# Kernel tuning notes

Hardware: AMD Instinct MI355X
Metric: run time of the kernel (lower is better)

The kernel has to match this reference:

```python
import jax, jax.numpy as jnp
import numpy as np

N_NODES, N_EDGES, N_GRAPHS = 100000, 400000, 4096
F_NODE, F_EDGE, G = 78, 11, 256
NUM_LAYERS, NUM_TIMESTEPS = 3, 2
L = NUM_LAYERS - 1  # number of GNNLayers after GetContext


def _lrelu(x):
    return jax.nn.leaky_relu(x, 0.01)


def _seg_softmax(logits, seg, n):
    # softmax of logits grouped by segment id (edge_softmax over dst / softmax_nodes over graph)
    m = jax.ops.segment_max(logits, seg, num_segments=n)
    e = jnp.exp(logits - m[seg])
    s = jax.ops.segment_sum(e, seg, num_segments=n)
    return e / s[seg]


def _gru(x, h, Wih, Whh, bih, bhh):
    gi = x @ Wih.T + bih
    gh = h @ Whh.T + bhh
    ir, iz, inn = jnp.split(gi, 3, axis=-1)
    hr, hz, hn = jnp.split(gh, 3, axis=-1)
    r = jax.nn.sigmoid(ir + hr)
    z = jax.nn.sigmoid(iz + hz)
    nn_ = jnp.tanh(inn + r * hn)
    return (1.0 - z) * nn_ + z * h


def _forward(node_feats, edge_feats, W_pn, b_pn, W_pe1, b_pe1, W_pe2, b_pe2, W_et, b_et,
             gru0_Wih, gru0_Whh, gru0_bih, gru0_bhh,
             gnn_W_pe, gnn_b_pe, gnn_W_pn, gnn_b_pn, gnn_Wih, gnn_Whh, gnn_bih, gnn_bhh,
             ro_W_cl, ro_b_cl, ro_W_pn, ro_b_pn, ro_Wih, ro_Whh, ro_bih, ro_bhh,
             ln_gamma, ln_beta, src, dst, node_graph):
    N, B = node_feats.shape[0], N_GRAPHS
    # ---- GetContext ----
    hv_new = _lrelu(node_feats @ W_pn.T + b_pn)                                  # [N,G]
    he1 = _lrelu(jnp.concatenate([node_feats[src], edge_feats], -1) @ W_pe1.T + b_pe1)  # [E,G]
    logits = _lrelu(jnp.concatenate([hv_new[dst], he1], -1) @ W_pe2.T + b_pe2)   # [E,1]
    a = _seg_softmax(logits, dst, N)
    c = jax.ops.segment_sum(a * (he1 @ W_et.T + b_et), dst, num_segments=N)      # [N,G]
    h = jax.nn.relu(_gru(jax.nn.elu(c), hv_new, gru0_Wih, gru0_Whh, gru0_bih, gru0_bhh))
    # ---- GNNLayers (AttentiveGRU2) ----
    for l in range(L):
        lg = _lrelu(jnp.concatenate([h[dst], h[src]], -1) @ gnn_W_pe[l].T + gnn_b_pe[l])  # [E,1]
        a = _seg_softmax(lg, dst, N)
        hv = h @ gnn_W_pn[l].T + gnn_b_pn[l]
        c = jax.ops.segment_sum(a * hv[src], dst, num_segments=N)
        h = jax.nn.relu(_gru(jax.nn.elu(c), h, gnn_Wih[l], gnn_Whh[l], gnn_bih[l], gnn_bhh[l]))
    # ---- AttentiveFPReadout ----
    g_feats = jax.ops.segment_sum(h, node_graph, num_segments=B)                 # [B,G]
    for t in range(NUM_TIMESTEPS):
        z = _lrelu(jnp.concatenate([jax.nn.relu(g_feats)[node_graph], h], -1) @ ro_W_cl[t].T + ro_b_cl[t])  # [N,1]
        a = _seg_softmax(z, node_graph, B)
        hv = h @ ro_W_pn[t].T + ro_b_pn[t]
        gr = jax.ops.segment_sum(a * hv, node_graph, num_segments=B)
        g_feats = jax.nn.relu(_gru(jax.nn.elu(gr), g_feats, ro_Wih[t], ro_Whh[t], ro_bih[t], ro_bhh[t]))
    # ---- LayerNorm (dropout is identity at inference) ----
    mu = jnp.mean(g_feats, -1, keepdims=True)
    var = jnp.mean((g_feats - mu) ** 2, -1, keepdims=True)
    return (g_feats - mu) / jnp.sqrt(var + 1e-5) * ln_gamma + ln_beta


def setup_inputs() -> dict:
    key = jax.random.key(0)
    ks = iter(jax.random.split(key, 64))

    def nrm(shape, scale=1.0):
        return jax.random.normal(next(ks), shape, dtype=jnp.float32) * scale

    def lin(out_d, in_d):
        return nrm((out_d, in_d), 1.0 / np.sqrt(in_d))

    d = {}
    d['node_feats'] = nrm((N_NODES, F_NODE))
    d['edge_feats'] = nrm((N_EDGES, F_EDGE))
    d['src'] = jax.random.randint(next(ks), (N_EDGES,), 0, N_NODES)
    d['dst'] = jax.random.randint(next(ks), (N_EDGES,), 0, N_NODES)
    d['node_graph'] = jnp.sort(jax.random.randint(next(ks), (N_NODES,), 0, N_GRAPHS))
    # GetContext params
    d['W_pn'] = lin(G, F_NODE); d['b_pn'] = jnp.zeros((G,), jnp.float32)
    d['W_pe1'] = lin(G, F_NODE + F_EDGE); d['b_pe1'] = jnp.zeros((G,), jnp.float32)
    d['W_pe2'] = lin(1, 2 * G); d['b_pe2'] = jnp.zeros((1,), jnp.float32)
    d['W_et'] = lin(G, G); d['b_et'] = jnp.zeros((G,), jnp.float32)
    d['gru0_Wih'] = lin(3 * G, G); d['gru0_Whh'] = lin(3 * G, G)
    d['gru0_bih'] = jnp.zeros((3 * G,), jnp.float32); d['gru0_bhh'] = jnp.zeros((3 * G,), jnp.float32)
    # stacked GNNLayer params
    s2g = 1.0 / np.sqrt(2 * G); sg = 1.0 / np.sqrt(G)
    d['gnn_W_pe'] = nrm((L, 1, 2 * G), s2g); d['gnn_b_pe'] = jnp.zeros((L, 1), jnp.float32)
    d['gnn_W_pn'] = nrm((L, G, G), sg); d['gnn_b_pn'] = jnp.zeros((L, G), jnp.float32)
    d['gnn_Wih'] = nrm((L, 3 * G, G), sg); d['gnn_Whh'] = nrm((L, 3 * G, G), sg)
    d['gnn_bih'] = jnp.zeros((L, 3 * G), jnp.float32); d['gnn_bhh'] = jnp.zeros((L, 3 * G), jnp.float32)
    # stacked readout (GlobalPool) params
    T = NUM_TIMESTEPS
    d['ro_W_cl'] = nrm((T, 1, 2 * G), s2g); d['ro_b_cl'] = jnp.zeros((T, 1), jnp.float32)
    d['ro_W_pn'] = nrm((T, G, G), sg); d['ro_b_pn'] = jnp.zeros((T, G), jnp.float32)
    d['ro_Wih'] = nrm((T, 3 * G, G), sg); d['ro_Whh'] = nrm((T, 3 * G, G), sg)
    d['ro_bih'] = jnp.zeros((T, 3 * G), jnp.float32); d['ro_bhh'] = jnp.zeros((T, 3 * G), jnp.float32)
    d['ln_gamma'] = jnp.ones((G,), jnp.float32); d['ln_beta'] = jnp.zeros((G,), jnp.float32)
    return d


def reference(node_feats, edge_feats, src, dst, node_graph, W_pn, b_pn, W_pe1, b_pe1, W_pe2, b_pe2,
              W_et, b_et, gru0_Wih, gru0_Whh, gru0_bih, gru0_bhh,
              gnn_W_pe, gnn_b_pe, gnn_W_pn, gnn_b_pn, gnn_Wih, gnn_Whh, gnn_bih, gnn_bhh,
              ro_W_cl, ro_b_cl, ro_W_pn, ro_b_pn, ro_Wih, ro_Whh, ro_bih, ro_bhh, ln_gamma, ln_beta):
    return _forward(node_feats, edge_feats, W_pn, b_pn, W_pe1, b_pe1, W_pe2, b_pe2, W_et, b_et,
                    gru0_Wih, gru0_Whh, gru0_bih, gru0_bhh,
                    gnn_W_pe, gnn_b_pe, gnn_W_pn, gnn_b_pn, gnn_Wih, gnn_Whh, gnn_bih, gnn_bhh,
                    ro_W_cl, ro_b_cl, ro_W_pn, ro_b_pn, ro_Wih, ro_Whh, ro_bih, ro_bhh,
                    ln_gamma, ln_beta, src, dst, node_graph)
```

## Files before the change

kernel.cpp:

```cpp
#include <hip/hip_runtime.h>

#define NN 100000
#define NE 400000
#define NB 4096
#define FN 78
#define FE 11
#define GD 256
#define NL 2
#define NT 2

typedef unsigned short u16;
typedef __attribute__((ext_vector_type(8))) short bf16x8;
typedef __attribute__((ext_vector_type(4))) float f32x4;

__device__ __forceinline__ float lrelu_(float x){ return x > 0.f ? x : 0.01f*x; }
__device__ __forceinline__ float elu_(float x){ return x > 0.f ? x : expf(x) - 1.f; }
__device__ __forceinline__ float sigm_(float x){ return 1.f/(1.f + expf(-x)); }

__device__ __forceinline__ float bf2f(u16 u){ return __uint_as_float(((unsigned)u) << 16); }
__device__ __forceinline__ u16 f2bf(float f){
  unsigned u = __float_as_uint(f);
  unsigned r = (u + 0x7fffu + ((u >> 16) & 1u)) >> 16;
  return (u16)r;
}
__device__ __forceinline__ float ldv(const float* p, size_t i){ return p[i]; }
__device__ __forceinline__ float ldv(const u16* p, size_t i){ return bf2f(p[i]); }
__device__ __forceinline__ void stv(float* p, size_t i, float v){ p[i] = v; }
__device__ __forceinline__ void stv(u16* p, size_t i, float v){ p[i] = f2bf(v); }

__global__ void k_zero(float* p, size_t n){
  size_t i = (size_t)blockIdx.x*blockDim.x + threadIdx.x;
  size_t st = (size_t)gridDim.x*blockDim.x;
  for (; i < n; i += st) p[i] = 0.f;
}

__global__ void k_count(const int* __restrict__ dst, int* __restrict__ cnt, int E){
  int e = blockIdx.x*256 + threadIdx.x;
  if (e < E) atomicAdd(&cnt[dst[e]], 1);
}
__global__ void k_scan1(const int* __restrict__ cnt, int* __restrict__ part,
                        int* __restrict__ btot, int n){
  __shared__ int sd[256];
  int i = blockIdx.x*256 + threadIdx.x;
  int v = (i < n) ? cnt[i] : 0;
  sd[threadIdx.x] = v; __syncthreads();
  for (int d=1; d<256; d<<=1){
    int t = (threadIdx.x >= d) ? sd[threadIdx.x-d] : 0;
    __syncthreads();
    sd[threadIdx.x] += t;
    __syncthreads();
  }
  if (i < n) part[i] = sd[threadIdx.x];
  if (threadIdx.x == 255) btot[blockIdx.x] = sd[255];
}
__global__ void k_scan2(const int* __restrict__ btot, int* __restrict__ boff, int nb){
  __shared__ int sd[512];
  int tid = threadIdx.x;
  int v = (tid < nb) ? btot[tid] : 0;
  sd[tid] = v; __syncthreads();
  for (int d=1; d<512; d<<=1){
    int t = (tid >= d) ? sd[tid-d] : 0;
    __syncthreads();
    sd[tid] += t;
    __syncthreads();
  }
  if (tid < nb) boff[tid] = sd[tid] - v;
}
__global__ void k_scan3(const int* __restrict__ part, const int* __restrict__ boff,
                        int* __restrict__ rowptr, int n){
  int i = blockIdx.x*256 + threadIdx.x;
  if (i < n) rowptr[i+1] = part[i] + boff[blockIdx.x];
  if (i == 0) rowptr[0] = 0;
}
__global__ void k_cursor(const int* __restrict__ rowptr, int* __restrict__ cursor, int n){
  int i = blockIdx.x*256 + threadIdx.x;
  if (i < n) cursor[i] = rowptr[i];
}
__global__ void k_fill(const int* __restrict__ dst, int* __restrict__ cursor,
                       int* __restrict__ order, int E){
  int e = blockIdx.x*256 + threadIdx.x;
  if (e < E){
    int pos = atomicAdd(&cursor[dst[e]], 1);
    order[pos] = e;
  }
}
__global__ void k_gpb(const int* __restrict__ ng, int* __restrict__ gpb, int N, int B){
  int b = blockIdx.x*256 + threadIdx.x;
  if (b > B) return;
  int lo = 0, hi = N;
  while (lo < hi){ int mid = (lo+hi)>>1; if (ng[mid] < b) lo = mid+1; else hi = mid; }
  gpb[b] = lo;
}

__global__ void k_pack_b(const float* __restrict__ W, u16* __restrict__ Bp, int OUT, int K){
  int t = blockIdx.x*256 + threadIdx.x;
  if (t >= OUT*K) return;
  int j = t & 7;
  int l = (t >> 3) & 63;
  int rest = t >> 9;
  int nks = K >> 5;
  int ks = rest % nks, c = rest / nks;
  int col = c*16 + (l & 15);
  int k = ks*32 + (l >> 4)*8 + j;
  Bp[t] = f2bf(W[(size_t)col*K + k]);
}

template<int TN>
__global__ void k_node_proj(const float* __restrict__ nf, const float* __restrict__ W, int ldw,
                            const float* __restrict__ b, int act, u16* __restrict__ outb, int N){
  __shared__ float sx[TN][FN];
  int base = blockIdx.x*TN, tid = threadIdx.x;
  for (int i = tid; i < TN*FN; i += 256){
    int n = i / FN, k = i % FN;
    int row = base + n;
    sx[n][k] = (row < N) ? nf[(size_t)row*FN + k] : 0.f;
  }
  __syncthreads();
  int j = tid;
  float acc[TN];
  #pragma unroll
  for (int n=0;n<TN;n++) acc[n]=0.f;
  for (int k=0;k<FN;k++){
    float w = W[(size_t)j*ldw + k];
    #pragma unroll
    for (int n=0;n<TN;n++) acc[n] += w*sx[n][k];
  }
  float bb = b ? b[j] : 0.f;
  #pragma unroll
  for (int n=0;n<TN;n++){
    int row = base + n;
    if (row < N){
      float v = acc[n] + bb;
      outb[(size_t)row*GD + j] = f2bf(act ? lrelu_(v) : v);
    }
  }
}

__global__ void k_dot2_bf16(const u16* __restrict__ rows, const float* __restrict__ wv,
                            float* __restrict__ za, float* __restrict__ zb, int N){
  int wav = threadIdx.x >> 6, lane = threadIdx.x & 63;
  int i = blockIdx.x*4 + wav;
  if (i >= N) return;
  int c0 = lane*4;
  ushort4 r4 = *(const ushort4*)&rows[(size_t)i*GD + c0];
  float4 wa = *(const float4*)&wv[c0];
  float4 wb = *(const float4*)&wv[GD + c0];
  float v0 = bf2f(r4.x), v1 = bf2f(r4.y), v2 = bf2f(r4.z), v3 = bf2f(r4.w);
  float va = v0*wa.x + v1*wa.y + v2*wa.z + v3*wa.w;
  float vb = v0*wb.x + v1*wb.y + v2*wb.z + v3*wb.w;
  #pragma unroll
  for (int off=32; off; off>>=1){ va += __shfl_down(va, off); vb += __shfl_down(vb, off); }
  if (lane == 0){ za[i] = va; zb[i] = vb; }
}

__global__ void k_dot1_bf16(const u16* __restrict__ rows, const float* __restrict__ wv,
                            float* __restrict__ z, int N){
  int wav = threadIdx.x >> 6, lane = threadIdx.x & 63;
  int i = blockIdx.x*4 + wav;
  if (i >= N) return;
  int c0 = lane*4;
  ushort4 r4 = *(const ushort4*)&rows[(size_t)i*GD + c0];
  float4 wa = *(const float4*)&wv[c0];
  float va = bf2f(r4.x)*wa.x + bf2f(r4.y)*wa.y + bf2f(r4.z)*wa.z + bf2f(r4.w)*wa.w;
  #pragma unroll
  for (int off=32; off; off>>=1) va += __shfl_down(va, off);
  if (lane == 0) z[i] = va;
}

__global__ void k_dotg_relu(const float* __restrict__ g, const float* __restrict__ wv,
                            float* __restrict__ zg, int B){
  int wav = threadIdx.x >> 6, lane = threadIdx.x & 63;
  int i = blockIdx.x*4 + wav;
  if (i >= B) return;
  int c0 = lane*4;
  float4 gv = *(const float4*)&g[(size_t)i*GD + c0];
  float4 wa = *(const float4*)&wv[c0];
  float va = fmaxf(gv.x,0.f)*wa.x + fmaxf(gv.y,0.f)*wa.y + fmaxf(gv.z,0.f)*wa.z + fmaxf(gv.w,0.f)*wa.w;
  #pragma unroll
  for (int off=32; off; off>>=1) va += __shfl_down(va, off);
  if (lane == 0) zg[i] = va;
}

__global__ void __launch_bounds__(256)
k_ctx_fused(const u16* __restrict__ P, const float* __restrict__ za,
            const int* __restrict__ order, const int* __restrict__ rowptr,
            const int* __restrict__ src, const float* __restrict__ ef,
            const float* __restrict__ Wpe1, const float* __restrict__ bpe1,
            const float* __restrict__ Wpe2, const float* __restrict__ bpe2,
            u16* __restrict__ wc, float* __restrict__ sdeg, int N){
  int wv = threadIdx.x >> 6, lane = threadIdx.x & 63;
  int d = blockIdx.x*4 + wv;
  if (d >= N) return;
  int j0 = rowptr[d], j1 = rowptr[d+1];
  int c0 = lane*4;
  float wb0 = Wpe2[GD+c0], wb1 = Wpe2[GD+c0+1], wb2 = Wpe2[GD+c0+2], wb3 = Wpe2[GD+c0+3];
  float bp0 = bpe1[c0], bp1 = bpe1[c0+1], bp2 = bpe1[c0+2], bp3 = bpe1[c0+3];
  float wk0[FE], wk1[FE], wk2[FE], wk3[FE];
  #pragma unroll
  for (int k=0;k<FE;k++){
    wk0[k] = Wpe1[(size_t)(c0+0)*(FN+FE) + FN + k];
    wk1[k] = Wpe1[(size_t)(c0+1)*(FN+FE) + FN + k];
    wk2[k] = Wpe1[(size_t)(c0+2)*(FN+FE) + FN + k];
    wk3[k] = Wpe1[(size_t)(c0+3)*(FN+FE) + FN + k];
  }
  float zad = za[d] + bpe2[0];
  float m = -1e30f, s = 0.f;
  float a0=0.f, a1=0.f, a2=0.f, a3=0.f;
  for (int j=j0; j<j1; j++){
    int e = order[j];
    int sn = src[e];
    ushort4 p4 = *(const ushort4*)&P[(size_t)sn*GD + c0];
    const float* efp = &ef[(size_t)e*FE];
    float efv[FE];
    #pragma unroll
    for (int k=0;k<FE;k++) efv[k] = efp[k];
    float h0 = bf2f(p4.x)+bp0, h1 = bf2f(p4.y)+bp1, h2 = bf2f(p4.z)+bp2, h3 = bf2f(p4.w)+bp3;
    #pragma unroll
    for (int k=0;k<FE;k++){
      h0 += wk0[k]*efv[k]; h1 += wk1[k]*efv[k]; h2 += wk2[k]*efv[k]; h3 += wk3[k]*efv[k];
    }
    h0 = lrelu_(h0); h1 = lrelu_(h1); h2 = lrelu_(h2); h3 = lrelu_(h3);
    float part = h0*wb0 + h1*wb1 + h2*wb2 + h3*wb3;
    #pragma unroll
    for (int off=32; off; off>>=1) part += __shfl_down(part, off);
    float l = lrelu_(part + zad);
    l = __shfl(l, 0);
    float mn = fmaxf(m, l);
    float sc = __expf(m - mn);
    float p  = __expf(l - mn);
    s = s*sc + p;
    a0 = a0*sc + p*h0; a1 = a1*sc + p*h1; a2 = a2*sc + p*h2; a3 = a3*sc + p*h3;
    m = mn;
  }
  float inv = (j1 > j0) ? 1.f/s : 0.f;
  ushort4 o;
  o.x = f2bf(a0*inv); o.y = f2bf(a1*inv); o.z = f2bf(a2*inv); o.w = f2bf(a3*inv);
  *(ushort4*)&wc[(size_t)d*GD + c0] = o;
  if (lane == 0) sdeg[d] = (j1 > j0) ? 1.f : 0.f;
}

__global__ void __launch_bounds__(256)
k_gnn_fused(const u16* __restrict__ hv, const float* __restrict__ za, const float* __restrict__ zb,
            const int* __restrict__ order, const int* __restrict__ rowptr,
            const int* __restrict__ src, const float* __restrict__ bias,
            u16* __restrict__ cw, int N){
  int wv = threadIdx.x >> 6, lane = threadIdx.x & 63;
  int d = blockIdx.x*4 + wv;
  if (d >= N) return;
  int j0 = rowptr[d], j1 = rowptr[d+1];
  int c0 = lane*4;
  float zad = za[d] + bias[0];
  float m = -1e30f, s = 0.f;
  float a0=0.f, a1=0.f, a2=0.f, a3=0.f;
  for (int j=j0; j<j1; j++){
    int e = order[j];
    int sn = src[e];
    float l = lrelu_(zad + zb[sn]);
    ushort4 r4 = *(const ushort4*)&hv[(size_t)sn*GD + c0];
    float mn = fmaxf(m, l);
    float sc = __expf(m - mn);
    float p  = __expf(l - mn);
    s = s*sc + p;
    a0 = a0*sc + p*bf2f(r4.x);
    a1 = a1*sc + p*bf2f(r4.y);
    a2 = a2*sc + p*bf2f(r4.z);
    a3 = a3*sc + p*bf2f(r4.w);
    m = mn;
  }
  float inv = (j1 > j0) ? 1.f/s : 0.f;
  ushort4 o;
  o.x = f2bf(a0*inv); o.y = f2bf(a1*inv); o.z = f2bf(a2*inv); o.w = f2bf(a3*inv);
  *(ushort4*)&cw[(size_t)d*GD + c0] = o;
}

__global__ void __launch_bounds__(256)
k_ro_fused(const u16* __restrict__ hv, const float* __restrict__ zg, const float* __restrict__ zh,
           const int* __restrict__ gpb, const float* __restrict__ bias,
           float* __restrict__ gr, int B){
  int b = blockIdx.x, tid = threadIdx.x;
  int i0 = gpb[b], i1 = gpb[b+1];
  float zgb = zg[b] + bias[0];
  __shared__ float red[256];
  float lm = -1e30f;
  for (int i = i0 + tid; i < i1; i += 256) lm = fmaxf(lm, lrelu_(zgb + zh[i]));
  red[tid] = lm; __syncthreads();
  for (int d2=128; d2; d2>>=1){ if (tid < d2) red[tid] = fmaxf(red[tid], red[tid+d2]); __syncthreads(); }
  float M = red[0]; __syncthreads();
  float ls = 0.f;
  for (int i = i0 + tid; i < i1; i += 256) ls += __expf(lrelu_(zgb + zh[i]) - M);
  red[tid] = ls; __syncthreads();
  for (int d2=128; d2; d2>>=1){ if (tid < d2) red[tid] += red[tid+d2]; __syncthreads(); }
  float S = red[0];
  float acc = 0.f;
  for (int i = i0; i < i1; i++){
    float p = __expf(lrelu_(zgb + zh[i]) - M);
    acc += p * bf2f(hv[(size_t)i*GD + tid]);
  }
  gr[(size_t)b*GD + tid] = (i1 > i0) ? acc/S : 0.f;
}

__global__ void k_segsum_sorted(const u16* __restrict__ h, const int* __restrict__ gpb,
                                float* __restrict__ g, int B){
  int b = blockIdx.x, tid = threadIdx.x;
  int i0 = gpb[b], i1 = gpb[b+1];
  float acc = 0.f;
  for (int i = i0; i < i1; i++) acc += bf2f(h[(size_t)i*GD + tid]);
  g[(size_t)b*GD + tid] = acc;
}

template<typename XT, typename HT, typename OT>
__global__ void __launch_bounds__(256)
k_gru_mfma(const XT* __restrict__ x, const HT* __restrict__ hprev,
           const u16* __restrict__ Wihp, const u16* __restrict__ Whhp,
           const float* __restrict__ bih, const float* __restrict__ bhh,
           OT* __restrict__ hout, int R, const float* __restrict__ xmask){
  int tid = threadIdx.x;
  int wave = tid >> 6, lane = tid & 63;
  int m = lane & 15, kg = lane >> 4;
  int r0 = blockIdx.x*16;

  f32x4 agi[3][4], agh[3][4];
  #pragma unroll
  for (int g=0;g<3;g++)
    #pragma unroll
    for (int t=0;t<4;t++){ agi[g][t] = (f32x4)(0.f); agh[g][t] = (f32x4)(0.f); }

  float mk = xmask ? (xmask[r0 + m] > 0.f ? 1.f : 0.f) : 1.f;
  #pragma unroll
  for (int ks=0; ks<8; ks++){
    int koff = ks*32 + kg*8;
    float xr[8];
    if constexpr (sizeof(XT) == 2){
      bf16x8 xw = *(const bf16x8*)&x[(size_t)(r0 + m)*GD + koff];
      #pragma unroll
      for (int q=0;q<8;q++) xr[q] = bf2f((u16)xw[q]);
    } else {
      const float* xp = (const float*)x + (size_t)(r0 + m)*GD + koff;
      float4 x0 = *(const float4*)xp;
      float4 x1 = *(const float4*)(xp+4);
      xr[0]=x0.x; xr[1]=x0.y; xr[2]=x0.z; xr[3]=x0.w;
      xr[4]=x1.x; xr[5]=x1.y; xr[6]=x1.z; xr[7]=x1.w;
    }
    bf16x8 ax;
    #pragma unroll
    for (int q=0;q<8;q++) ax[q] = (short)f2bf(elu_(xr[q]*mk));
    bf16x8 ah;
    if constexpr (sizeof(HT) == 2){
      ah = *(const bf16x8*)&hprev[(size_t)(r0 + m)*GD + koff];
    } else {
      const float* hr = (const float*)hprev + (size_t)(r0 + m)*GD + koff;
      float4 h0 = *(const float4*)hr;
      float4 h1 = *(const float4*)(hr+4);
      ah[0]=(short)f2bf(h0.x); ah[1]=(short)f2bf(h0.y); ah[2]=(short)f2bf(h0.z); ah[3]=(short)f2bf(h0.w);
      ah[4]=(short)f2bf(h1.x); ah[5]=(short)f2bf(h1.y); ah[6]=(short)f2bf(h1.z); ah[7]=(short)f2bf(h1.w);
    }
    #pragma unroll
    for (int g=0;g<3;g++){
      #pragma unroll
      for (int t=0;t<4;t++){
        int c = g*16 + wave*4 + t;
        bf16x8 bi = *(const bf16x8*)&Wihp[(size_t)((c*8 + ks)*64 + lane)*8];
        bf16x8 bh = *(const bf16x8*)&Whhp[(size_t)((c*8 + ks)*64 + lane)*8];
        agi[g][t] = __builtin_amdgcn_mfma_f32_16x16x32_bf16(ax, bi, agi[g][t], 0, 0, 0);
        agh[g][t] = __builtin_amdgcn_mfma_f32_16x16x32_bf16(ah, bh, agh[g][t], 0, 0, 0);
      }
    }
  }
  #pragma unroll
  for (int t=0;t<4;t++){
    int col = wave*64 + t*16 + m;
    float bir = bih[col],     bhr = bhh[col];
    float biz = bih[col+GD],  bhz = bhh[col+GD];
    float bin = bih[col+2*GD],bhn = bhh[col+2*GD];
    #pragma unroll
    for (int i=0;i<4;i++){
      int row = r0 + kg*4 + i;
      float rr = sigm_(agi[0][t][i] + bir + agh[0][t][i] + bhr);
      float zz = sigm_(agi[1][t][i] + biz + agh[1][t][i] + bhz);
      float nn = tanhf(agi[2][t][i] + bin + rr*(agh[2][t][i] + bhn));
      float hp = ldv(hprev, (size_t)row*GD + col);
      float o = (1.f - zz)*nn + zz*hp;
      stv(hout, (size_t)row*GD + col, fmaxf(o, 0.f));
    }
  }
}

__global__ void __launch_bounds__(256)
k_proj_mfma(const u16* __restrict__ X, const u16* __restrict__ Wp,
            const float* __restrict__ b, u16* __restrict__ Y, int R){
  int tid = threadIdx.x;
  int wave = tid >> 6, lane = tid & 63;
  int m = lane & 15, kg = lane >> 4;
  int r0 = blockIdx.x*32;
  f32x4 acc[2][4];
  #pragma unroll
  for (int rf=0;rf<2;rf++)
    #pragma unroll
    for (int t=0;t<4;t++) acc[rf][t] = (f32x4)(0.f);
  #pragma unroll
  for (int ks=0; ks<8; ks++){
    int koff = ks*32 + kg*8;
    bf16x8 a0 = *(const bf16x8*)&X[(size_t)(r0 + m)*GD + koff];
    bf16x8 a1 = *(const bf16x8*)&X[(size_t)(r0 + 16 + m)*GD + koff];
    #pragma unroll
    for (int t=0;t<4;t++){
      int c = wave*4 + t;
      bf16x8 bv = *(const bf16x8*)&Wp[(size_t)((c*8 + ks)*64 + lane)*8];
      acc[0][t] = __builtin_amdgcn_mfma_f32_16x16x32_bf16(a0, bv, acc[0][t], 0, 0, 0);
      acc[1][t] = __builtin_amdgcn_mfma_f32_16x16x32_bf16(a1, bv, acc[1][t], 0, 0, 0);
    }
  }
  #pragma unroll
  for (int t=0;t<4;t++){
    int col = wave*64 + t*16 + m;
    float bb = b[col];
    #pragma unroll
    for (int rf=0;rf<2;rf++){
      #pragma unroll
      for (int i=0;i<4;i++){
        int row = r0 + rf*16 + kg*4 + i;
        Y[(size_t)row*GD + col] = f2bf(acc[rf][t][i] + bb);
      }
    }
  }
}

__global__ void k_layernorm(const float* __restrict__ gb, const float* __restrict__ gamma,
                            const float* __restrict__ beta, float* __restrict__ outb){
  int r = blockIdx.x, j = threadIdx.x;
  float v = gb[(size_t)r*GD + j];
  float s1 = v, s2 = v*v;
  #pragma unroll
  for (int off=32; off; off>>=1){ s1 += __shfl_down(s1, off); s2 += __shfl_down(s2, off); }
  __shared__ float r1[4], r2[4];
  int wv = j >> 6, lane = j & 63;
  if (lane == 0){ r1[wv] = s1; r2[wv] = s2; }
  __syncthreads();
  float S1 = r1[0]+r1[1]+r1[2]+r1[3];
  float S2 = r2[0]+r2[1]+r2[2]+r2[3];
  float mu = S1/(float)GD;
  float var = fmaxf(S2/(float)GD - mu*mu, 0.f);
  outb[(size_t)r*GD + j] = (v - mu)/sqrtf(var + 1e-5f)*gamma[j] + beta[j];
}

extern "C" void kernel_launch(void* const* d_in, const int* in_sizes, int n_in,
                              void* d_out, int out_size, void* d_ws, size_t ws_size,
                              hipStream_t stream){
  const float* node_feats = (const float*)d_in[0];
  const float* edge_feats = (const float*)d_in[1];
  const int*   src        = (const int*)d_in[2];
  const int*   dst        = (const int*)d_in[3];
  const int*   node_graph = (const int*)d_in[4];
  const float* W_pn   = (const float*)d_in[5];
  const float* b_pn   = (const float*)d_in[6];
  const float* W_pe1  = (const float*)d_in[7];
  const float* b_pe1  = (const float*)d_in[8];
  const float* W_pe2  = (const float*)d_in[9];
  const float* b_pe2  = (const float*)d_in[10];
  const float* W_et   = (const float*)d_in[11];
  const float* b_et   = (const float*)d_in[12];
  const float* g0_Wih = (const float*)d_in[13];
  const float* g0_Whh = (const float*)d_in[14];
  const float* g0_bih = (const float*)d_in[15];
  const float* g0_bhh = (const float*)d_in[16];
  const float* gnn_W_pe = (const float*)d_in[17];
  const float* gnn_b_pe = (const float*)d_in[18];
  const float* gnn_W_pn = (const float*)d_in[19];
  const float* gnn_b_pn = (const float*)d_in[20];
  const float* gnn_Wih  = (const float*)d_in[21];
  const float* gnn_Whh  = (const float*)d_in[22];
  const float* gnn_bih  = (const float*)d_in[23];
  const float* gnn_bhh  = (const float*)d_in[24];
  const float* ro_W_cl = (const float*)d_in[25];
  const float* ro_b_cl = (const float*)d_in[26];
  const float* ro_W_pn = (const float*)d_in[27];
  const float* ro_b_pn = (const float*)d_in[28];
  const float* ro_Wih  = (const float*)d_in[29];
  const float* ro_Whh  = (const float*)d_in[30];
  const float* ro_bih  = (const float*)d_in[31];
  const float* ro_bhh  = (const float*)d_in[32];
  const float* ln_gamma = (const float*)d_in[33];
  const float* ln_beta  = (const float*)d_in[34];
  float* outp = (float*)d_out;

  const int NBLK = (NN + 255)/256;

  char* w = (char*)d_ws;
  size_t need = 0;
  float* gbuf  = (float*)(w + need); need += (size_t)NB*GD*4;
  float* grbuf = (float*)(w + need); need += (size_t)NB*GD*4;
  float* za    = (float*)(w + need); need += (size_t)NN*4;
  float* zb    = (float*)(w + need); need += (size_t)NN*4;
  float* zg    = (float*)(w + need); need += (size_t)NB*4;
  float* sdeg  = (float*)(w + need); need += (size_t)NN*4;
  int*   cnt    = (int*)(w + need); need += (size_t)NN*4;
  int*   rowptr = (int*)(w + need); need += (size_t)(NN+1)*4;
  int*   cursor = (int*)(w + need); need += (size_t)NN*4;
  int*   order  = (int*)(w + need); need += (size_t)NE*4;
  int*   gpb    = (int*)(w + need); need += (size_t)(NB+1)*4;
  int*   btot   = (int*)(w + need); need += (size_t)512*4;
  int*   boff   = (int*)(w + need); need += (size_t)512*4;
  u16*   hbuf = (u16*)(w + need); need += (size_t)NN*GD*2;
  u16*   htmp = (u16*)(w + need); need += (size_t)NN*GD*2;
  u16*   cwb  = (u16*)(w + need); need += (size_t)NN*GD*2;
  u16*   dbuf = (u16*)(w + need); need += (size_t)NN*GD*2;
  u16* pGru = (u16*)(w + need); need += (size_t)10*768*GD*2;
  u16* pPn  = (u16*)(w + need); need += (size_t)4*GD*GD*2;
  u16* pEt  = (u16*)(w + need); need += (size_t)GD*GD*2;
  if (ws_size < need) return;
  u16* Pbuf   = hbuf;
  u16* hv_new = htmp;

  const size_t GW = (size_t)768*GD;
  const size_t PW = (size_t)GD*GD;

  k_zero<<<64, 256, 0, stream>>>((float*)cnt, (size_t)NN);
  k_count<<<(NE+255)/256, 256, 0, stream>>>(dst, cnt, NE);
  k_scan1<<<NBLK, 256, 0, stream>>>(cnt, cnt, btot, NN);
  k_scan2<<<1, 512, 0, stream>>>(btot, boff, NBLK);
  k_scan3<<<NBLK, 256, 0, stream>>>(cnt, boff, rowptr, NN);
  k_cursor<<<NBLK, 256, 0, stream>>>(rowptr, cursor, NN);
  k_fill<<<(NE+255)/256, 256, 0, stream>>>(dst, cursor, order, NE);
  k_gpb<<<(NB+256)/256, 256, 0, stream>>>(node_graph, gpb, NN, NB);

  k_pack_b<<<768, 256, 0, stream>>>(g0_Wih, pGru + 0*GW, 768, GD);
  k_pack_b<<<768, 256, 0, stream>>>(g0_Whh, pGru + 1*GW, 768, GD);
  for (int l=0;l<NL;l++){
    k_pack_b<<<768, 256, 0, stream>>>(gnn_Wih + (size_t)l*3*GD*GD, pGru + (2+2*l)*GW, 768, GD);
    k_pack_b<<<768, 256, 0, stream>>>(gnn_Whh + (size_t)l*3*GD*GD, pGru + (3+2*l)*GW, 768, GD);
    k_pack_b<<<256, 256, 0, stream>>>(gnn_W_pn + (size_t)l*GD*GD, pPn + l*PW, GD, GD);
  }
  for (int t=0;t<NT;t++){
    k_pack_b<<<768, 256, 0, stream>>>(ro_Wih + (size_t)t*3*GD*GD, pGru + (6+2*t)*GW, 768, GD);
    k_pack_b<<<768, 256, 0, stream>>>(ro_Whh + (size_t)t*3*GD*GD, pGru + (7+2*t)*GW, 768, GD);
    k_pack_b<<<256, 256, 0, stream>>>(ro_W_pn + (size_t)t*GD*GD, pPn + (2+t)*PW, GD, GD);
  }
  k_pack_b<<<256, 256, 0, stream>>>(W_et, pEt, GD, GD);

  k_node_proj<8><<<(NN+7)/8, 256, 0, stream>>>(node_feats, W_pn, FN, b_pn, 1, hv_new, NN);
  k_node_proj<8><<<(NN+7)/8, 256, 0, stream>>>(node_feats, W_pe1, FN+FE, nullptr, 0, Pbuf, NN);
  k_dot1_bf16<<<(NN+3)/4, 256, 0, stream>>>(hv_new, W_pe2, za, NN);
  k_ctx_fused<<<(NN+3)/4, 256, 0, stream>>>(Pbuf, za, order, rowptr, src, edge_feats,
                                            W_pe1, b_pe1, W_pe2, b_pe2, cwb, sdeg, NN);
  k_proj_mfma<<<NN/32, 256, 0, stream>>>(cwb, pEt, b_et, dbuf, NN);
  k_gru_mfma<u16,u16,u16><<<NN/16, 256, 0, stream>>>(dbuf, hv_new, pGru + 0*GW, pGru + 1*GW,
                                                     g0_bih, g0_bhh, hbuf, NN, sdeg);

  for (int l=0; l<NL; l++){
    k_dot2_bf16<<<(NN+3)/4, 256, 0, stream>>>(hbuf, gnn_W_pe + (size_t)l*2*GD, za, zb, NN);
    k_proj_mfma<<<NN/32, 256, 0, stream>>>(hbuf, pPn + l*PW, gnn_b_pn + (size_t)l*GD, htmp, NN);
    k_gnn_fused<<<(NN+3)/4, 256, 0, stream>>>(htmp, za, zb, order, rowptr, src,
                                              gnn_b_pe + l, cwb, NN);
    k_gru_mfma<u16,u16,u16><<<NN/16, 256, 0, stream>>>(cwb, hbuf,
                                pGru + (2+2*l)*GW, pGru + (3+2*l)*GW,
                                gnn_bih + (size_t)l*3*GD, gnn_bhh + (size_t)l*3*GD, hbuf, NN, nullptr);
  }

  k_segsum_sorted<<<NB, 256, 0, stream>>>(hbuf, gpb, gbuf, NB);
  for (int t=0; t<NT; t++){
    k_dotg_relu<<<(NB+3)/4, 256, 0, stream>>>(gbuf, ro_W_cl + (size_t)t*2*GD, zg, NB);
    k_dot1_bf16<<<(NN+3)/4, 256, 0, stream>>>(hbuf, ro_W_cl + (size_t)t*2*GD + GD, za, NN);
    k_proj_mfma<<<NN/32, 256, 0, stream>>>(hbuf, pPn + (2+t)*PW, ro_b_pn + (size_t)t*GD, htmp, NN);
    k_ro_fused<<<NB, 256, 0, stream>>>(htmp, zg, za, gpb, ro_b_cl + t, grbuf, NB);
    k_gru_mfma<float,float,float><<<NB/16, 256, 0, stream>>>(grbuf, gbuf,
                                pGru + (6+2*t)*GW, pGru + (7+2*t)*GW,
                                ro_bih + (size_t)t*3*GD, ro_bhh + (size_t)t*3*GD, gbuf, NB, nullptr);
  }
  k_layernorm<<<NB, 256, 0, stream>>>(gbuf, ln_gamma, ln_beta, outp);
}
```

Measured before the change: 2.220 ms.

## Tile GRU and projection MFMA kernels to 64 rows and move ELU into producers

The node-level GRU and projection kernels now process 64 rows per 512-thread block instead of 16 or 32, so each loaded weight fragment feeds four row-tile MFMAs rather than one or two. This is meant to cut repeated weight reads from cache, which were issued once per small block. The ELU (and the degree mask on the context path) moves out of the GRU prologue into the epilogues that produce its input: the GNN aggregation kernel and a templated projection kernel. The trade-off is many more accumulator registers per thread, which may limit occupancy or cause spills, and the last partial tile is handled by clamping reads and guarding writes.

```diff
diff --git a/kernel.cpp b/kernel.cpp
--- a/kernel.cpp
+++ b/kernel.cpp
@@ -23,10 +23,6 @@
   unsigned r = (u + 0x7fffu + ((u >> 16) & 1u)) >> 16;
   return (u16)r;
 }
-__device__ __forceinline__ float ldv(const float* p, size_t i){ return p[i]; }
-__device__ __forceinline__ float ldv(const u16* p, size_t i){ return bf2f(p[i]); }
-__device__ __forceinline__ void stv(float* p, size_t i, float v){ p[i] = v; }
-__device__ __forceinline__ void stv(u16* p, size_t i, float v){ p[i] = f2bf(v); }
 
 __global__ void k_zero(float* p, size_t n){
   size_t i = (size_t)blockIdx.x*blockDim.x + threadIdx.x;
@@ -269,7 +265,8 @@
   }
   float inv = (j1 > j0) ? 1.f/s : 0.f;
   ushort4 o;
-  o.x = f2bf(a0*inv); o.y = f2bf(a1*inv); o.z = f2bf(a2*inv); o.w = f2bf(a3*inv);
+  o.x = f2bf(elu_(a0*inv)); o.y = f2bf(elu_(a1*inv));
+  o.z = f2bf(elu_(a2*inv)); o.w = f2bf(elu_(a3*inv));
   *(ushort4*)&cw[(size_t)d*GD + c0] = o;
 }
 
@@ -308,12 +305,134 @@
   g[(size_t)b*GD + tid] = acc;
 }
 
-template<typename XT, typename HT, typename OT>
+__global__ void __launch_bounds__(512)
+k_gru_mfma64(const u16* __restrict__ x, const u16* __restrict__ hprev,
+             const u16* __restrict__ Wihp, const u16* __restrict__ Whhp,
+             const float* __restrict__ bih, const float* __restrict__ bhh,
+             u16* __restrict__ hout, int R){
+  int tid = threadIdx.x;
+  int wv = tid >> 6, lane = tid & 63;
+  int m = lane & 15, kg = lane >> 4;
+  int r0 = blockIdx.x*64;
+
+  f32x4 agi[3][2][4], agh[3][2][4];
+  #pragma unroll
+  for (int g=0;g<3;g++)
+    #pragma unroll
+    for (int t=0;t<2;t++)
+      #pragma unroll
+      for (int rt=0;rt<4;rt++){ agi[g][t][rt] = (f32x4)(0.f); agh[g][t][rt] = (f32x4)(0.f); }
+
+  #pragma unroll
+  for (int ks=0; ks<8; ks++){
+    int koff = ks*32 + kg*8;
+    bf16x8 ax[4], ah[4];
+    #pragma unroll
+    for (int rt=0; rt<4; rt++){
+      int row = r0 + rt*16 + m;
+      if (row > R-1) row = R-1;
+      ax[rt] = *(const bf16x8*)&x[(size_t)row*GD + koff];
+      ah[rt] = *(const bf16x8*)&hprev[(size_t)row*GD + koff];
+    }
+    #pragma unroll
+    for (int g=0;g<3;g++){
+      #pragma unroll
+      for (int t=0;t<2;t++){
+        int c = g*16 + wv*2 + t;
+        bf16x8 bi = *(const bf16x8*)&Wihp[(size_t)((c*8 + ks)*64 + lane)*8];
+        bf16x8 bh = *(const bf16x8*)&Whhp[(size_t)((c*8 + ks)*64 + lane)*8];
+        #pragma unroll
+        for (int rt=0; rt<4; rt++){
+          agi[g][t][rt] = __builtin_amdgcn_mfma_f32_16x16x32_bf16(ax[rt], bi, agi[g][t][rt], 0, 0, 0);
+          agh[g][t][rt] = __builtin_amdgcn_mfma_f32_16x16x32_bf16(ah[rt], bh, agh[g][t][rt], 0, 0, 0);
+        }
+      }
+    }
+  }
+  #pragma unroll
+  for (int t=0;t<2;t++){
+    int col = wv*32 + t*16 + m;
+    float bir = bih[col],      bhr = bhh[col];
+    float biz = bih[col+GD],   bhz = bhh[col+GD];
+    float bin = bih[col+2*GD], bhn = bhh[col+2*GD];
+    #pragma unroll
+    for (int rt=0; rt<4; rt++){
+      #pragma unroll
+      for (int i=0;i<4;i++){
+        int row = r0 + rt*16 + kg*4 + i;
+        if (row < R){
+          float rr = sigm_(agi[0][t][rt][i] + bir + agh[0][t][rt][i] + bhr);
+          float zz = sigm_(agi[1][t][rt][i] + biz + agh[1][t][rt][i] + bhz);
+          float nn = tanhf(agi[2][t][rt][i] + bin + rr*(agh[2][t][rt][i] + bhn));
+          float hp = bf2f(hprev[(size_t)row*GD + col]);
+          float o = (1.f - zz)*nn + zz*hp;
+          hout[(size_t)row*GD + col] = f2bf(fmaxf(o, 0.f));
+        }
+      }
+    }
+  }
+}
+
+template<int DO_ELU>
+__global__ void __launch_bounds__(512)
+k_proj_mfma64(const u16* __restrict__ X, const u16* __restrict__ Wp,
+              const float* __restrict__ b, u16* __restrict__ Y, int R,
+              const float* __restrict__ mask){
+  int tid = threadIdx.x;
+  int wv = tid >> 6, lane = tid & 63;
+  int m = lane & 15, kg = lane >> 4;
+  int r0 = blockIdx.x*64;
+  f32x4 acc[2][4];
+  #pragma unroll
+  for (int t=0;t<2;t++)
+    #pragma unroll
+    for (int rt=0;rt<4;rt++) acc[t][rt] = (f32x4)(0.f);
+  #pragma unroll
+  for (int ks=0; ks<8; ks++){
+    int koff = ks*32 + kg*8;
+    bf16x8 a[4];
+    #pragma unroll
+    for (int rt=0; rt<4; rt++){
+      int row = r0 + rt*16 + m;
+      if (row > R-1) row = R-1;
+      a[rt] = *(const bf16x8*)&X[(size_t)row*GD + koff];
+    }
+    #pragma unroll
+    for (int t=0;t<2;t++){
+      int c = wv*2 + t;
+      bf16x8 bv = *(const bf16x8*)&Wp[(size_t)((c*8 + ks)*64 + lane)*8];
+      #pragma unroll
+      for (int rt=0; rt<4; rt++)
+        acc[t][rt] = __builtin_amdgcn_mfma_f32_16x16x32_bf16(a[rt], bv, acc[t][rt], 0, 0, 0);
+    }
+  }
+  #pragma unroll
+  for (int t=0;t<2;t++){
+    int col = wv*32 + t*16 + m;
+    float bb = b[col];
+    #pragma unroll
+    for (int rt=0; rt<4; rt++){
+      #pragma unroll
+      for (int i=0;i<4;i++){
+        int row = r0 + rt*16 + kg*4 + i;
+        if (row < R){
+          float v = acc[t][rt][i] + bb;
+          if (DO_ELU){
+            float mk = (mask[row] > 0.f) ? 1.f : 0.f;
+            v = elu_(v*mk);
+          }
+          Y[(size_t)row*GD + col] = f2bf(v);
+        }
+      }
+    }
+  }
+}
+
 __global__ void __launch_bounds__(256)
-k_gru_mfma(const XT* __restrict__ x, const HT* __restrict__ hprev,
-           const u16* __restrict__ Wihp, const u16* __restrict__ Whhp,
-           const float* __restrict__ bih, const float* __restrict__ bhh,
-           OT* __restrict__ hout, int R, const float* __restrict__ xmask){
+k_gru_mfma_f32(const float* __restrict__ x, const float* __restrict__ hprev,
+               const u16* __restrict__ Wihp, const u16* __restrict__ Whhp,
+               const float* __restrict__ bih, const float* __restrict__ bhh,
+               float* __restrict__ hout, int R){
   int tid = threadIdx.x;
   int wave = tid >> 6, lane = tid & 63;
   int m = lane & 15, kg = lane >> 4;
@@ -325,35 +444,23 @@
     #pragma unroll
     for (int t=0;t<4;t++){ agi[g][t] = (f32x4)(0.f); agh[g][t] = (f32x4)(0.f); }
 
-  float mk = xmask ? (xmask[r0 + m] > 0.f ? 1.f : 0.f) : 1.f;
   #pragma unroll
   for (int ks=0; ks<8; ks++){
     int koff = ks*32 + kg*8;
-    float xr[8];
-    if constexpr (sizeof(XT) == 2){
-      bf16x8 xw = *(const bf16x8*)&x[(size_t)(r0 + m)*GD + koff];
-      #pragma unroll
-      for (int q=0;q<8;q++) xr[q] = bf2f((u16)xw[q]);
-    } else {
-      const float* xp = (const float*)x + (size_t)(r0 + m)*GD + koff;
-      float4 x0 = *(const float4*)xp;
-      float4 x1 = *(const float4*)(xp+4);
-      xr[0]=x0.x; xr[1]=x0.y; xr[2]=x0.z; xr[3]=x0.w;
-      xr[4]=x1.x; xr[5]=x1.y; xr[6]=x1.z; xr[7]=x1.w;
-    }
+    const float* xp = x + (size_t)(r0 + m)*GD + koff;
+    float4 x0 = *(const float4*)xp;
+    float4 x1 = *(const float4*)(xp+4);
     bf16x8 ax;
-    #pragma unroll
-    for (int q=0;q<8;q++) ax[q] = (short)f2bf(elu_(xr[q]*mk));
+    ax[0]=(short)f2bf(elu_(x0.x)); ax[1]=(short)f2bf(elu_(x0.y));
+    ax[2]=(short)f2bf(elu_(x0.z)); ax[3]=(short)f2bf(elu_(x0.w));
+    ax[4]=(short)f2bf(elu_(x1.x)); ax[5]=(short)f2bf(elu_(x1.y));
+    ax[6]=(short)f2bf(elu_(x1.z)); ax[7]=(short)f2bf(elu_(x1.w));
+    const float* hr = hprev + (size_t)(r0 + m)*GD + koff;
+    float4 h0 = *(const float4*)hr;
+    float4 h1 = *(const float4*)(hr+4);
     bf16x8 ah;
-    if constexpr (sizeof(HT) == 2){
-      ah = *(const bf16x8*)&hprev[(size_t)(r0 + m)*GD + koff];
-    } else {
-      const float* hr = (const float*)hprev + (size_t)(r0 + m)*GD + koff;
-      float4 h0 = *(const float4*)hr;
-      float4 h1 = *(const float4*)(hr+4);
-      ah[0]=(short)f2bf(h0.x); ah[1]=(short)f2bf(h0.y); ah[2]=(short)f2bf(h0.z); ah[3]=(short)f2bf(h0.w);
-      ah[4]=(short)f2bf(h1.x); ah[5]=(short)f2bf(h1.y); ah[6]=(short)f2bf(h1.z); ah[7]=(short)f2bf(h1.w);
-    }
+    ah[0]=(short)f2bf(h0.x); ah[1]=(short)f2bf(h0.y); ah[2]=(short)f2bf(h0.z); ah[3]=(short)f2bf(h0.w);
+    ah[4]=(short)f2bf(h1.x); ah[5]=(short)f2bf(h1.y); ah[6]=(short)f2bf(h1.z); ah[7]=(short)f2bf(h1.w);
     #pragma unroll
     for (int g=0;g<3;g++){
       #pragma unroll
@@ -369,58 +476,18 @@
   #pragma unroll
   for (int t=0;t<4;t++){
     int col = wave*64 + t*16 + m;
-    float bir = bih[col],     bhr = bhh[col];
-    float biz = bih[col+GD],  bhz = bhh[col+GD];
-    float bin = bih[col+2*GD],bhn = bhh[col+2*GD];
+    float bir = bih[col],      bhr = bhh[col];
+    float biz = bih[col+GD],   bhz = bhh[col+GD];
+    float bin = bih[col+2*GD], bhn = bhh[col+2*GD];
     #pragma unroll
     for (int i=0;i<4;i++){
       int row = r0 + kg*4 + i;
       float rr = sigm_(agi[0][t][i] + bir + agh[0][t][i] + bhr);
       float zz = sigm_(agi[1][t][i] + biz + agh[1][t][i] + bhz);
       float nn = tanhf(agi[2][t][i] + bin + rr*(agh[2][t][i] + bhn));
-      float hp = ldv(hprev, (size_t)row*GD + col);
+      float hp = hprev[(size_t)row*GD + col];
       float o = (1.f - zz)*nn + zz*hp;
-      stv(hout, (size_t)row*GD + col, fmaxf(o, 0.f));
-    }
-  }
-}
-
-__global__ void __launch_bounds__(256)
-k_proj_mfma(const u16* __restrict__ X, const u16* __restrict__ Wp,
-            const float* __restrict__ b, u16* __restrict__ Y, int R){
-  int tid = threadIdx.x;
-  int wave = tid >> 6, lane = tid & 63;
-  int m = lane & 15, kg = lane >> 4;
-  int r0 = blockIdx.x*32;
-  f32x4 acc[2][4];
-  #pragma unroll
-  for (int rf=0;rf<2;rf++)
-    #pragma unroll
-    for (int t=0;t<4;t++) acc[rf][t] = (f32x4)(0.f);
-  #pragma unroll
-  for (int ks=0; ks<8; ks++){
-    int koff = ks*32 + kg*8;
-    bf16x8 a0 = *(const bf16x8*)&X[(size_t)(r0 + m)*GD + koff];
-    bf16x8 a1 = *(const bf16x8*)&X[(size_t)(r0 + 16 + m)*GD + koff];
-    #pragma unroll
-    for (int t=0;t<4;t++){
-      int c = wave*4 + t;
-      bf16x8 bv = *(const bf16x8*)&Wp[(size_t)((c*8 + ks)*64 + lane)*8];
-      acc[0][t] = __builtin_amdgcn_mfma_f32_16x16x32_bf16(a0, bv, acc[0][t], 0, 0, 0);
-      acc[1][t] = __builtin_amdgcn_mfma_f32_16x16x32_bf16(a1, bv, acc[1][t], 0, 0, 0);
-    }
-  }
-  #pragma unroll
-  for (int t=0;t<4;t++){
-    int col = wave*64 + t*16 + m;
-    float bb = b[col];
-    #pragma unroll
-    for (int rf=0;rf<2;rf++){
-      #pragma unroll
-      for (int i=0;i<4;i++){
-        int row = r0 + rf*16 + kg*4 + i;
-        Y[(size_t)row*GD + col] = f2bf(acc[rf][t][i] + bb);
-      }
+      hout[(size_t)row*GD + col] = fmaxf(o, 0.f);
     }
   }
 }
@@ -513,6 +580,7 @@
 
   const size_t GW = (size_t)768*GD;
   const size_t PW = (size_t)GD*GD;
+  const int G64 = (NN + 63)/64;
 
   k_zero<<<64, 256, 0, stream>>>((float*)cnt, (size_t)NN);
   k_count<<<(NE+255)/256, 256, 0, stream>>>(dst, cnt, NE);
@@ -542,29 +610,31 @@
   k_dot1_bf16<<<(NN+3)/4, 256, 0, stream>>>(hv_new, W_pe2, za, NN);
   k_ctx_fused<<<(NN+3)/4, 256, 0, stream>>>(Pbuf, za, order, rowptr, src, edge_feats,
                                             W_pe1, b_pe1, W_pe2, b_pe2, cwb, sdeg, NN);
-  k_proj_mfma<<<NN/32, 256, 0, stream>>>(cwb, pEt, b_et, dbuf, NN);
-  k_gru_mfma<u16,u16,u16><<<NN/16, 256, 0, stream>>>(dbuf, hv_new, pGru + 0*GW, pGru + 1*GW,
-                                                     g0_bih, g0_bhh, hbuf, NN, sdeg);
+  k_proj_mfma64<1><<<G64, 512, 0, stream>>>(cwb, pEt, b_et, dbuf, NN, sdeg);
+  k_gru_mfma64<<<G64, 512, 0, stream>>>(dbuf, hv_new, pGru + 0*GW, pGru + 1*GW,
+                                        g0_bih, g0_bhh, hbuf, NN);
 
   for (int l=0; l<NL; l++){
     k_dot2_bf16<<<(NN+3)/4, 256, 0, stream>>>(hbuf, gnn_W_pe + (size_t)l*2*GD, za, zb, NN);
-    k_proj_mfma<<<NN/32, 256, 0, stream>>>(hbuf, pPn + l*PW, gnn_b_pn + (size_t)l*GD, htmp, NN);
+    k_proj_mfma64<0><<<G64, 512, 0, stream>>>(hbuf, pPn + l*PW, gnn_b_pn + (size_t)l*GD,
+                                              htmp, NN, nullptr);
     k_gnn_fused<<<(NN+3)/4, 256, 0, stream>>>(htmp, za, zb, order, rowptr, src,
                                               gnn_b_pe + l, cwb, NN);
-    k_gru_mfma<u16,u16,u16><<<NN/16, 256, 0, stream>>>(cwb, hbuf,
+    k_gru_mfma64<<<G64, 512, 0, stream>>>(cwb, hbuf,
                                 pGru + (2+2*l)*GW, pGru + (3+2*l)*GW,
-                                gnn_bih + (size_t)l*3*GD, gnn_bhh + (size_t)l*3*GD, hbuf, NN, nullptr);
+                                gnn_bih + (size_t)l*3*GD, gnn_bhh + (size_t)l*3*GD, hbuf, NN);
   }
 
   k_segsum_sorted<<<NB, 256, 0, stream>>>(hbuf, gpb, gbuf, NB);
   for (int t=0; t<NT; t++){
     k_dotg_relu<<<(NB+3)/4, 256, 0, stream>>>(gbuf, ro_W_cl + (size_t)t*2*GD, zg, NB);
     k_dot1_bf16<<<(NN+3)/4, 256, 0, stream>>>(hbuf, ro_W_cl + (size_t)t*2*GD + GD, za, NN);
-    k_proj_mfma<<<NN/32, 256, 0, stream>>>(hbuf, pPn + (2+t)*PW, ro_b_pn + (size_t)t*GD, htmp, NN);
+    k_proj_mfma64<0><<<G64, 512, 0, stream>>>(hbuf, pPn + (2+t)*PW, ro_b_pn + (size_t)t*GD,
+                                              htmp, NN, nullptr);
     k_ro_fused<<<NB, 256, 0, stream>>>(htmp, zg, za, gpb, ro_b_cl + t, grbuf, NB);
-    k_gru_mfma<float,float,float><<<NB/16, 256, 0, stream>>>(grbuf, gbuf,
+    k_gru_mfma_f32<<<NB/16, 256, 0, stream>>>(grbuf, gbuf,
                                 pGru + (6+2*t)*GW, pGru + (7+2*t)*GW,
-                                ro_bih + (size_t)t*3*GD, ro_bhh + (size_t)t*3*GD, gbuf, NB, nullptr);
+                                ro_bih + (size_t)t*3*GD, ro_bhh + (size_t)t*3*GD, gbuf, NB);
   }
   k_layernorm<<<NB, 256, 0, stream>>>(gbuf, ln_gamma, ln_beta, outp);
 }
```

Result: slower. 2.962 ms (+33.4%).
